# Kernel tuning notes

Hardware: AMD Instinct MI355X
Metric: run time of the kernel (lower is better)

## Reference

```python
import jax, jax.numpy as jnp
import numpy as np

DIM = 1024
NUM_HEADS = 16
HEAD_DIM = DIM // NUM_HEADS
BINDING_BIAS = 0.5
SCALE = HEAD_DIM ** -0.5


def setup_inputs() -> dict:
    key = jax.random.key(0)
    ks = jax.random.split(key, 10)
    B, S, D = 2, 2048, DIM
    std = D ** -0.5
    return {
        "x": jax.random.normal(ks[0], (B, S, D), jnp.float32),
        "binding_matrix": jax.random.uniform(ks[1], (S, S), jnp.float32),
        "Wq": jax.random.normal(ks[2], (D, D), jnp.float32) * std,
        "bq": jnp.zeros((D,), jnp.float32),
        "Wk": jax.random.normal(ks[3], (D, D), jnp.float32) * std,
        "bk": jnp.zeros((D,), jnp.float32),
        "Wv": jax.random.normal(ks[4], (D, D), jnp.float32) * std,
        "bv": jnp.zeros((D,), jnp.float32),
        "Wo": jax.random.normal(ks[5], (D, D), jnp.float32) * std,
        "bo": jnp.zeros((D,), jnp.float32),
    }


def reference(x, binding_matrix, Wq, bq, Wk, bk, Wv, bv, Wo, bo):
    B, S, D = x.shape
    H, Hd = NUM_HEADS, HEAD_DIM
    # projections -> [B, H, S, Hd]
    q = (x @ Wq + bq).reshape(B, S, H, Hd).transpose(0, 2, 1, 3)
    k = (x @ Wk + bk).reshape(B, S, H, Hd).transpose(0, 2, 1, 3)
    v = (x @ Wv + bv).reshape(B, S, H, Hd).transpose(0, 2, 1, 3)
    # scores [B, H, S, S] with additive binding bias
    attn = jnp.einsum("bhqd,bhkd->bhqk", q, k) * SCALE
    attn = attn + BINDING_BIAS * binding_matrix[None, None, :, :]
    attn = jax.nn.softmax(attn, axis=-1)
    out = jnp.einsum("bhqk,bhkd->bhqd", attn, v)
    out = out.transpose(0, 2, 1, 3).reshape(B, S, D)
    return out @ Wo + bo
```

## Files before the change

### kernel.cpp

```cpp
#include <hip/hip_runtime.h>

#define DEV static __device__ __forceinline__

typedef __attribute__((ext_vector_type(4))) float f32x4;
typedef __attribute__((ext_vector_type(8))) __bf16 bfv8;
typedef __attribute__((ext_vector_type(8))) short s8v;
typedef __attribute__((ext_vector_type(4))) short s4v;

DEV short f2bf(float f) {
    unsigned u = __float_as_uint(f);
    u = (u + 0x7fffu + ((u >> 16) & 1u)) >> 16;
    return (short)u;
}
DEV float bf2f(short s) { return __uint_as_float(((unsigned)(unsigned short)s) << 16); }

DEV void gload16(const void* g, void* l) {
    __builtin_amdgcn_global_load_lds(
        (const __attribute__((address_space(1))) void*)g,
        (__attribute__((address_space(3))) void*)l, 16, 0, 0);
}

DEV f32x4 mfma16(bfv8 a, bfv8 b, f32x4 c) {
    return __builtin_amdgcn_mfma_f32_16x16x32_bf16(a, b, c, 0, 0, 0);
}

DEV float max3f(float a, float b, float c) {
    float d;
    asm("v_max3_f32 %0, %1, %2, %3" : "=v"(d) : "v"(a), "v"(b), "v"(c));
    return d;
}
DEV unsigned cvtpk(float lo, float hi) {
    unsigned w;
    asm("v_cvt_pk_bf16_f32 %0, %1, %2" : "=v"(w) : "v"(lo), "v"(hi));
    return w;
}

DEV bfv8 ldsfrag(const short* base, int row, int slog) {
    int sp = slog ^ (row & 7);
    return *reinterpret_cast<const bfv8*>(base + row * 64 + sp * 8);
}

__global__ void k_cvt(const float* __restrict__ in, short* __restrict__ out, float s) {
    int i = blockIdx.x * blockDim.x + threadIdx.x;
    const float4* p = (const float4*)in + (size_t)i * 2;
    float4 a = p[0], b = p[1];
    s8v o;
    o[0] = f2bf(a.x * s); o[1] = f2bf(a.y * s); o[2] = f2bf(a.z * s); o[3] = f2bf(a.w * s);
    o[4] = f2bf(b.x * s); o[5] = f2bf(b.y * s); o[6] = f2bf(b.z * s); o[7] = f2bf(b.w * s);
    reinterpret_cast<s8v*>(out)[i] = o;
}

__global__ void k_cvtb(const float* __restrict__ in, short* __restrict__ out, float s) {
    int i = blockIdx.x * blockDim.x + threadIdx.x;
    int ktn = i >> 11, q = i & 2047;
    const float4* p = reinterpret_cast<const float4*>(in + (size_t)q * 2048 + ktn * 16);
    float4 a = p[0], b = p[1], cc = p[2], d = p[3];
    s8v o0, o1;
    o0[0] = f2bf(a.x * s); o0[1] = f2bf(a.y * s); o0[2] = f2bf(a.z * s); o0[3] = f2bf(a.w * s);
    o0[4] = f2bf(b.x * s); o0[5] = f2bf(b.y * s); o0[6] = f2bf(b.z * s); o0[7] = f2bf(b.w * s);
    o1[0] = f2bf(cc.x * s); o1[1] = f2bf(cc.y * s); o1[2] = f2bf(cc.z * s); o1[3] = f2bf(cc.w * s);
    o1[4] = f2bf(d.x * s); o1[5] = f2bf(d.y * s); o1[6] = f2bf(d.z * s); o1[7] = f2bf(d.w * s);
    s8v* dst = reinterpret_cast<s8v*>(out + (size_t)i * 16);
    dst[0] = o0; dst[1] = o1;
}

__global__ void k_transpose4(
    const float* __restrict__ W0, const float* __restrict__ W1,
    const float* __restrict__ W2, const float* __restrict__ W3,
    short* __restrict__ T0, short* __restrict__ T1,
    short* __restrict__ T2, short* __restrict__ T3, float s0)
{
    __shared__ float tl[32][33];
    const int z = blockIdx.z;
    const float* W = z == 0 ? W0 : z == 1 ? W1 : z == 2 ? W2 : W3;
    short* Wt = z == 0 ? T0 : z == 1 ? T1 : z == 2 ? T2 : T3;
    const float s = z == 0 ? s0 : 1.f;
    int tx = threadIdx.x & 31, ty = threadIdx.x >> 5;
    int nb = blockIdx.x * 32, kb = blockIdx.y * 32;
#pragma unroll
    for (int i = 0; i < 4; i++)
        tl[ty + i * 8][tx] = W[(kb + ty + i * 8) * 1024 + nb + tx];
    __syncthreads();
#pragma unroll
    for (int i = 0; i < 4; i++)
        Wt[(nb + ty + i * 8) * 1024 + kb + tx] = f2bf(tl[tx][ty + i * 8] * s);
}

template <int EPI>
DEV void gemm_store(f32x4 a4, int gr, int gc, const float* bias, float bscale,
                    void* outp)
{
    const float bvl = bias[gc] * bscale;
    const int h = gc >> 6, d = gc & 63;
    if (EPI == 2) {
        float* O = (float*)outp;
#pragma unroll
        for (int r = 0; r < 4; r++) O[(gr + r) * 1024 + gc] = a4[r] + bvl;
    } else {
        const int b = gr >> 11, sr = gr & 2047;
        short* O = (short*)outp;
        if (EPI == 0) {
            int base = ((b * 16 + h) * 2048 + sr) * 64 + d;
#pragma unroll
            for (int r = 0; r < 4; r++) O[base + r * 64] = f2bf(a4[r] + bvl);
        } else {
            s4v vv;
#pragma unroll
            for (int r = 0; r < 4; r++) vv[r] = f2bf(a4[r] + bvl);
            const int s6 = sr & 63;
            const int qp = (sr & ~63) | (s6 & 35) | ((s6 & 12) << 1) | ((s6 & 16) >> 2);
            *reinterpret_cast<s4v*>(O + ((b * 16 + h) * 64 + d) * 2048 + qp) = vv;
        }
    }
}

template <int EPI>
DEV void gemm_body(const short* __restrict__ A, const short* __restrict__ Bt,
                   const float* __restrict__ bias, void* __restrict__ outp,
                   float bscale, int row0, int col0, short* As, short* Bs)
{
    const int t = threadIdx.x, lane = t & 63;
    const int wv = t >> 6, wr = wv >> 1, wc = wv & 1;
    const int g = lane >> 4, c = lane & 15;

    const f32x4 z4 = {0.f, 0.f, 0.f, 0.f};
    f32x4 acc[2][4];
#pragma unroll
    for (int m = 0; m < 2; m++)
#pragma unroll
        for (int n = 0; n < 4; n++) acc[m][n] = z4;

    for (int kt = 0; kt < 16; ++kt) {
        const int k0 = kt * 64;
        const short* Ag = A + row0 * 1024 + k0;
        const short* Bg = Bt + col0 * 1024 + k0;
#pragma unroll
        for (int j = 0; j < 2; j++) {
            int idx = j * 256 + t;
            int row = idx >> 3, sp = idx & 7, sl = sp ^ (row & 7);
            gload16(Ag + row * 1024 + sl * 8, As + idx * 8);
        }
#pragma unroll
        for (int j = 0; j < 4; j++) {
            int idx = j * 256 + t;
            int row = idx >> 3, sp = idx & 7, sl = sp ^ (row & 7);
            gload16(Bg + row * 1024 + sl * 8, Bs + idx * 8);
        }
        __syncthreads();

        bfv8 af[2][2], bfr[4][2];
#pragma unroll
        for (int m = 0; m < 2; m++)
#pragma unroll
            for (int ks = 0; ks < 2; ks++)
                af[m][ks] = ldsfrag(As, wr * 32 + m * 16 + c, ks * 4 + g);
#pragma unroll
        for (int n = 0; n < 4; n++)
#pragma unroll
            for (int ks = 0; ks < 2; ks++)
                bfr[n][ks] = ldsfrag(Bs, wc * 64 + n * 16 + c, ks * 4 + g);
        __builtin_amdgcn_s_setprio(1);
#pragma unroll
        for (int m = 0; m < 2; m++)
#pragma unroll
            for (int n = 0; n < 4; n++)
#pragma unroll
                for (int ks = 0; ks < 2; ks++)
                    acc[m][n] = mfma16(af[m][ks], bfr[n][ks], acc[m][n]);
        __builtin_amdgcn_s_setprio(0);
        __syncthreads();
    }

#pragma unroll
    for (int n = 0; n < 4; n++) {
        const int gc = col0 + wc * 64 + n * 16 + c;
#pragma unroll
        for (int m = 0; m < 2; m++)
            gemm_store<EPI>(acc[m][n], row0 + wr * 32 + m * 16 + g * 4, gc,
                            bias, bscale, outp);
    }
}

template <int EPI>
DEV void gemm_body128(const short* __restrict__ A, const short* __restrict__ Bt,
                      const float* __restrict__ bias, void* __restrict__ outp,
                      float bscale, int row0, int col0, short* As, short* Bs)
{
    const int t = threadIdx.x, lane = t & 63;
    const int wv = t >> 6, wr = wv >> 1, wc = wv & 1;
    const int g = lane >> 4, c = lane & 15;

    const f32x4 z4 = {0.f, 0.f, 0.f, 0.f};
    f32x4 acc[4][4];
#pragma unroll
    for (int m = 0; m < 4; m++)
#pragma unroll
        for (int n = 0; n < 4; n++) acc[m][n] = z4;

    for (int kt = 0; kt < 16; ++kt) {
        const int k0 = kt * 64;
        const short* Ag = A + row0 * 1024 + k0;
        const short* Bg = Bt + col0 * 1024 + k0;
#pragma unroll
        for (int j = 0; j < 4; j++) {
            int idx = j * 256 + t;
            int row = idx >> 3, sp = idx & 7, sl = sp ^ (row & 7);
            gload16(Ag + row * 1024 + sl * 8, As + idx * 8);
            gload16(Bg + row * 1024 + sl * 8, Bs + idx * 8);
        }
        __syncthreads();

        bfv8 af[4][2], bfr[4][2];
#pragma unroll
        for (int m = 0; m < 4; m++)
#pragma unroll
            for (int ks = 0; ks < 2; ks++)
                af[m][ks] = ldsfrag(As, wr * 64 + m * 16 + c, ks * 4 + g);
#pragma unroll
        for (int n = 0; n < 4; n++)
#pragma unroll
            for (int ks = 0; ks < 2; ks++)
                bfr[n][ks] = ldsfrag(Bs, wc * 64 + n * 16 + c, ks * 4 + g);
        __builtin_amdgcn_s_setprio(1);
#pragma unroll
        for (int m = 0; m < 4; m++)
#pragma unroll
            for (int n = 0; n < 4; n++)
#pragma unroll
                for (int ks = 0; ks < 2; ks++)
                    acc[m][n] = mfma16(af[m][ks], bfr[n][ks], acc[m][n]);
        __builtin_amdgcn_s_setprio(0);
        __syncthreads();
    }

#pragma unroll
    for (int n = 0; n < 4; n++) {
        const int gc = col0 + wc * 64 + n * 16 + c;
#pragma unroll
        for (int m = 0; m < 4; m++)
            gemm_store<EPI>(acc[m][n], row0 + wr * 64 + m * 16 + g * 4, gc,
                            bias, bscale, outp);
    }
}

__global__ __launch_bounds__(256, 2) void k_gemm3(
    const short* __restrict__ A,
    const short* __restrict__ WqT, const short* __restrict__ WkT, const short* __restrict__ WvT,
    const float* __restrict__ bq, const float* __restrict__ bk, const float* __restrict__ bv,
    short* __restrict__ Qs, short* __restrict__ Kst, short* __restrict__ Vts, float scq)
{
    __shared__ alignas(16) short As[128 * 64];
    __shared__ alignas(16) short Bs[128 * 64];
    const int which = blockIdx.y >> 3;
    const int col0 = (blockIdx.y & 7) * 128;
    const int row0 = blockIdx.x * 128;
    if (which == 0)
        gemm_body128<0>(A, WqT, bq, Qs, scq, row0, col0, As, Bs);
    else if (which == 1)
        gemm_body128<0>(A, WkT, bk, Kst, 1.f, row0, col0, As, Bs);
    else
        gemm_body128<1>(A, WvT, bv, Vts, 1.f, row0, col0, As, Bs);
}

__global__ __launch_bounds__(256, 2) void k_gemmO(
    const short* __restrict__ A, const short* __restrict__ Bt,
    const float* __restrict__ bias, float* __restrict__ outp)
{
    __shared__ alignas(16) short As[64 * 64];
    __shared__ alignas(16) short Bs[128 * 64];
    gemm_body<2>(A, Bt, bias, outp, 1.f, blockIdx.x * 64, blockIdx.y * 128, As, Bs);
}

__global__ __launch_bounds__(1024, 4) void k_attn(
    const short* __restrict__ Q, const short* __restrict__ K,
    const short* __restrict__ Vt, const short* __restrict__ bbt,
    short* __restrict__ Ob)
{
    __shared__ alignas(16) short Ks[2][64 * 64];
    __shared__ alignas(16) short Vs[2][64 * 64];
    const int t = threadIdx.x, lane = t & 63;
    const int wv = t >> 6, g = lane >> 4, c = lane & 15;
    const int qt = blockIdx.x, bh = blockIdx.y;
    const int b = bh >> 4, h = bh & 15;
    const short* Qb = Q + bh * 2048 * 64;
    const short* Kb = K + bh * 2048 * 64;
    const short* Vb = Vt + bh * 64 * 2048;
    const int q0 = qt * 256 + wv * 16;

    bfv8 qf[2];
#pragma unroll
    for (int ks = 0; ks < 2; ks++)
        qf[ks] = *reinterpret_cast<const bfv8*>(Qb + (q0 + c) * 64 + ks * 32 + g * 8);

    const f32x4 z4 = {0.f, 0.f, 0.f, 0.f};
    f32x4 oa[4];
#pragma unroll
    for (int nd = 0; nd < 4; nd++) oa[nd] = z4;
    f32x4 lacc = z4;
    float mrun = 20.0f;

    s8v ob_;
#pragma unroll
    for (int i = 0; i < 8; i++) ob_[i] = (short)0x3F80;
    const bfv8 ones = __builtin_bit_cast(bfv8, ob_);

    const bool isK = t < 512;
    const int sidx = isK ? t : t - 512;
    const int srow = sidx >> 3, ssl = ((sidx & 7) ^ (srow & 7)) * 8;
    const short* sp_ = isK ? (Kb + srow * 64 + ssl) : (Vb + srow * 2048 + ssl);
    const int sinc = isK ? 4096 : 64;
    const int dst8 = sidx * 8;
    const short* bbp = bbt + (size_t)(q0 + c) * 16 + 4 * g;

    const int cx = c & 7;
    const int fofs0 = c * 128 + ((g ^ cx) << 4);
    const int fofs1 = c * 128 + (((4 + g) ^ cx) << 4);

    gload16(sp_, isK ? &Ks[0][dst8] : &Vs[0][dst8]);
    sp_ += sinc;
    s4v bn[4];
#pragma unroll
    for (int n = 0; n < 4; n++)
        bn[n] = *reinterpret_cast<const s4v*>(bbp + n * 32768);
    bbp += 131072;
    __syncthreads();

    for (int kt = 0; kt < 32; ++kt) {
        const int cur = kt & 1;
        f32x4 cb[4];
#pragma unroll
        for (int n = 0; n < 4; n++)
#pragma unroll
            for (int r = 0; r < 4; r++) cb[n][r] = bf2f(bn[n][r]);
        if (kt < 31) {
            const int nb = cur ^ 1;
            gload16(sp_, isK ? &Ks[nb][dst8] : &Vs[nb][dst8]);
            sp_ += sinc;
#pragma unroll
            for (int n = 0; n < 4; n++)
                bn[n] = *reinterpret_cast<const s4v*>(bbp + n * 32768);
            bbp += 131072;
        }

        const char* Kc = (const char*)&Ks[cur][0];
        const char* Vc = (const char*)&Vs[cur][0];

        f32x4 sc[4];
        __builtin_amdgcn_s_setprio(1);
#pragma unroll
        for (int n = 0; n < 4; n++) {
            bfv8 k0 = *reinterpret_cast<const bfv8*>(Kc + fofs0 + n * 2048);
            bfv8 k1 = *reinterpret_cast<const bfv8*>(Kc + fofs1 + n * 2048);
            sc[n] = mfma16(k0, qf[0], cb[n]);
            sc[n] = mfma16(k1, qf[1], sc[n]);
        }
        __builtin_amdgcn_s_setprio(0);

#pragma unroll
        for (int n = 0; n < 4; n++)
#pragma unroll
            for (int r = 0; r < 4; r++)
                sc[n][r] = __builtin_amdgcn_exp2f(sc[n][r] - mrun);

        unsigned w0[4], w1[4];
#pragma unroll
        for (int n = 0; n < 4; n++) {
            w0[n] = cvtpk(sc[n][0], sc[n][1]);
            w1[n] = cvtpk(sc[n][2], sc[n][3]);
        }
        typedef struct { unsigned a, b, c2, d; } u4;
        u4 q0w; q0w.a = w0[0]; q0w.b = w1[0]; q0w.c2 = w0[1]; q0w.d = w1[1];
        u4 q1w; q1w.a = w0[2]; q1w.b = w1[2]; q1w.c2 = w0[3]; q1w.d = w1[3];
        const bfv8 pf0 = __builtin_bit_cast(bfv8, q0w);
        const bfv8 pf1 = __builtin_bit_cast(bfv8, q1w);

        __builtin_amdgcn_s_setprio(1);
#pragma unroll
        for (int nd = 0; nd < 4; nd++) {
            bfv8 v0 = *reinterpret_cast<const bfv8*>(Vc + fofs0 + nd * 2048);
            bfv8 v1 = *reinterpret_cast<const bfv8*>(Vc + fofs1 + nd * 2048);
            oa[nd] = mfma16(v0, pf0, oa[nd]);
            oa[nd] = mfma16(v1, pf1, oa[nd]);
        }
        lacc = mfma16(ones, pf0, lacc);
        lacc = mfma16(ones, pf1, lacc);
        __builtin_amdgcn_s_setprio(0);

        float t0 = fmaxf(max3f(sc[0][0], sc[0][1], sc[0][2]), sc[0][3]);
        float t1 = fmaxf(max3f(sc[1][0], sc[1][1], sc[1][2]), sc[1][3]);
        float t2 = fmaxf(max3f(sc[2][0], sc[2][1], sc[2][2]), sc[2][3]);
        float t3 = fmaxf(max3f(sc[3][0], sc[3][1], sc[3][2]), sc[3][3]);
        float pemax = fmaxf(max3f(t0, t1, t2), t3);
        if (!__all(pemax <= 2896.0f)) {
            float rmax = fmaxf(pemax, __shfl_xor(pemax, 16));
            rmax = fmaxf(rmax, __shfl_xor(rmax, 32));
            if (rmax > 2896.0f) {
                const float corr = 1.0f / rmax;
                mrun += __log2f(rmax);
#pragma unroll
                for (int nd = 0; nd < 4; nd++)
#pragma unroll
                    for (int r = 0; r < 4; r++) oa[nd][r] *= corr;
#pragma unroll
                for (int r = 0; r < 4; r++) lacc[r] *= corr;
            }
        }
        __syncthreads();
    }

    const float rl = 1.0f / lacc[0];
    const size_t orow = (size_t)(b * 2048 + q0 + c);
#pragma unroll
    for (int nd = 0; nd < 4; nd++) {
        s4v st;
#pragma unroll
        for (int r = 0; r < 4; r++) st[r] = f2bf(oa[nd][r] * rl);
        *reinterpret_cast<s4v*>(Ob + orow * 1024 + h * 64 + nd * 16 + 4 * g) = st;
    }
}

extern "C" void kernel_launch(void* const* d_in, const int* in_sizes, int n_in,
                              void* d_out, int out_size, void* d_ws, size_t ws_size,
                              hipStream_t stream)
{
    (void)in_sizes; (void)n_in; (void)out_size; (void)ws_size;
    const float* x    = (const float*)d_in[0];
    const float* bind = (const float*)d_in[1];
    const float* Wq   = (const float*)d_in[2];
    const float* bq   = (const float*)d_in[3];
    const float* Wk   = (const float*)d_in[4];
    const float* bk   = (const float*)d_in[5];
    const float* Wv   = (const float*)d_in[6];
    const float* bv   = (const float*)d_in[7];
    const float* Wo   = (const float*)d_in[8];
    const float* bo   = (const float*)d_in[9];

    char* ws = (char*)d_ws;
    const size_t MB = (size_t)1 << 20;
    short* xb   = (short*)(ws + 0 * MB);
    short* Wqt  = (short*)(ws + 8 * MB);
    short* Wkt  = (short*)(ws + 10 * MB);
    short* Wvt  = (short*)(ws + 12 * MB);
    short* Wot  = (short*)(ws + 14 * MB);
    short* bbm  = (short*)(ws + 16 * MB);
    short* Qs   = (short*)(ws + 24 * MB);
    short* Kst  = (short*)(ws + 32 * MB);
    short* Vts  = (short*)(ws + 40 * MB);
    short* Obuf = (short*)(ws + 48 * MB);

    const float LOG2E = 1.4426950408889634f;
    const float SCQ = 0.125f * LOG2E;
    const float SCB = 0.5f * LOG2E;

    k_cvt<<<2048, 256, 0, stream>>>(x, xb, 1.f);
    k_cvtb<<<1024, 256, 0, stream>>>(bind, bbm, SCB);
    k_transpose4<<<dim3(32, 32, 4), 256, 0, stream>>>(Wq, Wk, Wv, Wo,
                                                      Wqt, Wkt, Wvt, Wot, SCQ);
    k_gemm3<<<dim3(32, 24), 256, 0, stream>>>(xb, Wqt, Wkt, Wvt, bq, bk, bv,
                                              Qs, Kst, Vts, SCQ);
    k_attn<<<dim3(8, 32), 1024, 0, stream>>>(Qs, Kst, Vts, bbm, Obuf);
    k_gemmO<<<dim3(64, 8), 256, 0, stream>>>(Obuf, Wot, bo, (float*)d_out);
}
```

Before: 122.0 us.

## Double attention key tile to 128 and split K/V loads across all threads

The attention loop now handles 128 keys per iteration instead of 64, halving the iteration count and the number of block-wide barriers. Every thread now issues one K and one V global-to-LDS load per tile, instead of half the threads loading K and half loading V. The V shared-memory layout and swizzled fragment offsets are reworked for the wider tile. In exchange, LDS use doubles to 64KB per block and each thread holds more score and bias registers, which may lower occupancy or cause spills given the 1024-thread launch bound.

```diff
diff --git a/kernel.cpp b/kernel.cpp
--- a/kernel.cpp
+++ b/kernel.cpp
@@ -276,8 +276,8 @@
     const short* __restrict__ Vt, const short* __restrict__ bbt,
     short* __restrict__ Ob)
 {
-    __shared__ alignas(16) short Ks[2][64 * 64];
-    __shared__ alignas(16) short Vs[2][64 * 64];
+    __shared__ alignas(16) short Ks[2][128 * 64];
+    __shared__ alignas(16) short Vs[2][64 * 128];
     const int t = threadIdx.x, lane = t & 63;
     const int wv = t >> 6, g = lane >> 4, c = lane & 15;
     const int qt = blockIdx.x, bh = blockIdx.y;
@@ -304,93 +304,101 @@
     for (int i = 0; i < 8; i++) ob_[i] = (short)0x3F80;
     const bfv8 ones = __builtin_bit_cast(bfv8, ob_);
 
-    const bool isK = t < 512;
-    const int sidx = isK ? t : t - 512;
-    const int srow = sidx >> 3, ssl = ((sidx & 7) ^ (srow & 7)) * 8;
-    const short* sp_ = isK ? (Kb + srow * 64 + ssl) : (Vb + srow * 2048 + ssl);
-    const int sinc = isK ? 4096 : 64;
-    const int dst8 = sidx * 8;
+    const int krow = t >> 3, ksl = ((t & 7) ^ (krow & 7)) * 8;
+    const short* kp0 = Kb + krow * 64 + ksl;
+    const int vrow = t >> 4, vp_ = t & 15;
+    const int vcol = ((vp_ >> 3) * 8 + ((vp_ & 7) ^ (vrow & 7))) * 8;
+    const short* vp0 = Vb + vrow * 2048 + vcol;
+    const int dst8 = t * 8;
     const short* bbp = bbt + (size_t)(q0 + c) * 16 + 4 * g;
 
     const int cx = c & 7;
-    const int fofs0 = c * 128 + ((g ^ cx) << 4);
-    const int fofs1 = c * 128 + (((4 + g) ^ cx) << 4);
-
-    gload16(sp_, isK ? &Ks[0][dst8] : &Vs[0][dst8]);
-    sp_ += sinc;
-    s4v bn[4];
-#pragma unroll
-    for (int n = 0; n < 4; n++)
+    const int kofs0 = c * 128 + ((g ^ cx) << 4);
+    const int kofs1 = c * 128 + (((4 + g) ^ cx) << 4);
+    int vofs[4];
+#pragma unroll
+    for (int j = 0; j < 4; j++)
+        vofs[j] = c * 256 + (((((j & 1) * 4 + g) ^ cx) + 8 * (j >> 1)) << 4);
+
+    gload16(kp0, &Ks[0][dst8]);
+    gload16(vp0, &Vs[0][dst8]);
+    kp0 += 8192; vp0 += 128;
+    s4v bn[8];
+#pragma unroll
+    for (int n = 0; n < 8; n++)
         bn[n] = *reinterpret_cast<const s4v*>(bbp + n * 32768);
-    bbp += 131072;
+    bbp += 262144;
     __syncthreads();
 
-    for (int kt = 0; kt < 32; ++kt) {
+    for (int kt = 0; kt < 16; ++kt) {
         const int cur = kt & 1;
-        f32x4 cb[4];
-#pragma unroll
-        for (int n = 0; n < 4; n++)
-#pragma unroll
-            for (int r = 0; r < 4; r++) cb[n][r] = bf2f(bn[n][r]);
-        if (kt < 31) {
+        const char* Kc = (const char*)&Ks[cur][0];
+        f32x4 sc[8];
+        __builtin_amdgcn_s_setprio(1);
+#pragma unroll
+        for (int n = 0; n < 8; n++) {
+            f32x4 cb;
+#pragma unroll
+            for (int r = 0; r < 4; r++) cb[r] = bf2f(bn[n][r]);
+            bfv8 k0 = *reinterpret_cast<const bfv8*>(Kc + kofs0 + n * 2048);
+            bfv8 k1 = *reinterpret_cast<const bfv8*>(Kc + kofs1 + n * 2048);
+            sc[n] = mfma16(k0, qf[0], cb);
+            sc[n] = mfma16(k1, qf[1], sc[n]);
+        }
+        __builtin_amdgcn_s_setprio(0);
+
+        if (kt < 15) {
             const int nb = cur ^ 1;
-            gload16(sp_, isK ? &Ks[nb][dst8] : &Vs[nb][dst8]);
-            sp_ += sinc;
-#pragma unroll
-            for (int n = 0; n < 4; n++)
+            gload16(kp0, &Ks[nb][dst8]);
+            gload16(vp0, &Vs[nb][dst8]);
+            kp0 += 8192; vp0 += 128;
+#pragma unroll
+            for (int n = 0; n < 8; n++)
                 bn[n] = *reinterpret_cast<const s4v*>(bbp + n * 32768);
-            bbp += 131072;
-        }
-
-        const char* Kc = (const char*)&Ks[cur][0];
-        const char* Vc = (const char*)&Vs[cur][0];
-
-        f32x4 sc[4];
-        __builtin_amdgcn_s_setprio(1);
-#pragma unroll
-        for (int n = 0; n < 4; n++) {
-            bfv8 k0 = *reinterpret_cast<const bfv8*>(Kc + fofs0 + n * 2048);
-            bfv8 k1 = *reinterpret_cast<const bfv8*>(Kc + fofs1 + n * 2048);
-            sc[n] = mfma16(k0, qf[0], cb[n]);
-            sc[n] = mfma16(k1, qf[1], sc[n]);
-        }
-        __builtin_amdgcn_s_setprio(0);
-
-#pragma unroll
-        for (int n = 0; n < 4; n++)
+            bbp += 262144;
+        }
+
+#pragma unroll
+        for (int n = 0; n < 8; n++)
 #pragma unroll
             for (int r = 0; r < 4; r++)
                 sc[n][r] = __builtin_amdgcn_exp2f(sc[n][r] - mrun);
 
-        unsigned w0[4], w1[4];
-#pragma unroll
-        for (int n = 0; n < 4; n++) {
+        unsigned w0[8], w1[8];
+#pragma unroll
+        for (int n = 0; n < 8; n++) {
             w0[n] = cvtpk(sc[n][0], sc[n][1]);
             w1[n] = cvtpk(sc[n][2], sc[n][3]);
         }
         typedef struct { unsigned a, b, c2, d; } u4;
-        u4 q0w; q0w.a = w0[0]; q0w.b = w1[0]; q0w.c2 = w0[1]; q0w.d = w1[1];
-        u4 q1w; q1w.a = w0[2]; q1w.b = w1[2]; q1w.c2 = w0[3]; q1w.d = w1[3];
-        const bfv8 pf0 = __builtin_bit_cast(bfv8, q0w);
-        const bfv8 pf1 = __builtin_bit_cast(bfv8, q1w);
-
+        bfv8 pf[4];
+#pragma unroll
+        for (int j = 0; j < 4; j++) {
+            u4 qw; qw.a = w0[2 * j]; qw.b = w1[2 * j];
+            qw.c2 = w0[2 * j + 1]; qw.d = w1[2 * j + 1];
+            pf[j] = __builtin_bit_cast(bfv8, qw);
+        }
+
+        const char* Vc = (const char*)&Vs[cur][0];
         __builtin_amdgcn_s_setprio(1);
 #pragma unroll
         for (int nd = 0; nd < 4; nd++) {
-            bfv8 v0 = *reinterpret_cast<const bfv8*>(Vc + fofs0 + nd * 2048);
-            bfv8 v1 = *reinterpret_cast<const bfv8*>(Vc + fofs1 + nd * 2048);
-            oa[nd] = mfma16(v0, pf0, oa[nd]);
-            oa[nd] = mfma16(v1, pf1, oa[nd]);
-        }
-        lacc = mfma16(ones, pf0, lacc);
-        lacc = mfma16(ones, pf1, lacc);
+#pragma unroll
+            for (int j = 0; j < 4; j++) {
+                bfv8 vf = *reinterpret_cast<const bfv8*>(Vc + vofs[j] + nd * 4096);
+                oa[nd] = mfma16(vf, pf[j], oa[nd]);
+            }
+        }
+#pragma unroll
+        for (int j = 0; j < 4; j++) lacc = mfma16(ones, pf[j], lacc);
         __builtin_amdgcn_s_setprio(0);
 
-        float t0 = fmaxf(max3f(sc[0][0], sc[0][1], sc[0][2]), sc[0][3]);
-        float t1 = fmaxf(max3f(sc[1][0], sc[1][1], sc[1][2]), sc[1][3]);
-        float t2 = fmaxf(max3f(sc[2][0], sc[2][1], sc[2][2]), sc[2][3]);
-        float t3 = fmaxf(max3f(sc[3][0], sc[3][1], sc[3][2]), sc[3][3]);
-        float pemax = fmaxf(max3f(t0, t1, t2), t3);
+        float pemax = 0.f;
+#pragma unroll
+        for (int n = 0; n < 8; n++) {
+            float tn = fmaxf(max3f(sc[n][0], sc[n][1], sc[n][2]), sc[n][3]);
+            pemax = fmaxf(pemax, tn);
+        }
         if (!__all(pemax <= 2896.0f)) {
             float rmax = fmaxf(pemax, __shfl_xor(pemax, 16));
             rmax = fmaxf(rmax, __shfl_xor(rmax, 32));
```

New measurement: 123.6 us. About the same (+1.4%).

## Double-buffer LDS tiles in projection GEMMs to overlap loads with MFMA

Applied to the files above, without the earlier changes.

Both GEMM bodies (QKV projection and output projection) now use two LDS buffers per operand. The next K-tile is prefetched with global_load_lds while MFMAs run on the current tile, and per-thread source pointers are precomputed and advanced instead of recomputed each iteration. This is meant to hide global-load latency behind compute. In exchange it doubles the GEMM kernels' shared-memory footprint, which may limit how many blocks fit per CU.

```diff
diff --git a/kernel.cpp b/kernel.cpp
--- a/kernel.cpp
+++ b/kernel.cpp
@@ -117,7 +117,8 @@
 template <int EPI>
 DEV void gemm_body(const short* __restrict__ A, const short* __restrict__ Bt,
                    const float* __restrict__ bias, void* __restrict__ outp,
-                   float bscale, int row0, int col0, short* As, short* Bs)
+                   float bscale, int row0, int col0, short (*As)[64 * 64],
+                   short (*Bs)[128 * 64])
 {
     const int t = threadIdx.x, lane = t & 63;
     const int wv = t >> 6, wr = wv >> 1, wc = wv & 1;
@@ -130,35 +131,46 @@
 #pragma unroll
         for (int n = 0; n < 4; n++) acc[m][n] = z4;
 
+    const short* Ap[2]; const short* Bp[4]; int Ad[2], Bd[4];
+#pragma unroll
+    for (int j = 0; j < 2; j++) {
+        int idx = j * 256 + t;
+        int row = idx >> 3, sl = ((idx & 7) ^ (row & 7)) * 8;
+        Ap[j] = A + row0 * 1024 + row * 1024 + sl;
+        Ad[j] = idx * 8;
+    }
+#pragma unroll
+    for (int j = 0; j < 4; j++) {
+        int idx = j * 256 + t;
+        int row = idx >> 3, sl = ((idx & 7) ^ (row & 7)) * 8;
+        Bp[j] = Bt + col0 * 1024 + row * 1024 + sl;
+        Bd[j] = idx * 8;
+    }
+    auto stage = [&](int buf) {
+#pragma unroll
+        for (int j = 0; j < 2; j++) { gload16(Ap[j], &As[buf][Ad[j]]); Ap[j] += 64; }
+#pragma unroll
+        for (int j = 0; j < 4; j++) { gload16(Bp[j], &Bs[buf][Bd[j]]); Bp[j] += 64; }
+    };
+
+    stage(0);
+    __syncthreads();
+
     for (int kt = 0; kt < 16; ++kt) {
-        const int k0 = kt * 64;
-        const short* Ag = A + row0 * 1024 + k0;
-        const short* Bg = Bt + col0 * 1024 + k0;
-#pragma unroll
-        for (int j = 0; j < 2; j++) {
-            int idx = j * 256 + t;
-            int row = idx >> 3, sp = idx & 7, sl = sp ^ (row & 7);
-            gload16(Ag + row * 1024 + sl * 8, As + idx * 8);
-        }
-#pragma unroll
-        for (int j = 0; j < 4; j++) {
-            int idx = j * 256 + t;
-            int row = idx >> 3, sp = idx & 7, sl = sp ^ (row & 7);
-            gload16(Bg + row * 1024 + sl * 8, Bs + idx * 8);
-        }
-        __syncthreads();
+        const int cur = kt & 1;
+        if (kt < 15) stage(cur ^ 1);
 
         bfv8 af[2][2], bfr[4][2];
 #pragma unroll
         for (int m = 0; m < 2; m++)
 #pragma unroll
             for (int ks = 0; ks < 2; ks++)
-                af[m][ks] = ldsfrag(As, wr * 32 + m * 16 + c, ks * 4 + g);
+                af[m][ks] = ldsfrag(As[cur], wr * 32 + m * 16 + c, ks * 4 + g);
 #pragma unroll
         for (int n = 0; n < 4; n++)
 #pragma unroll
             for (int ks = 0; ks < 2; ks++)
-                bfr[n][ks] = ldsfrag(Bs, wc * 64 + n * 16 + c, ks * 4 + g);
+                bfr[n][ks] = ldsfrag(Bs[cur], wc * 64 + n * 16 + c, ks * 4 + g);
         __builtin_amdgcn_s_setprio(1);
 #pragma unroll
         for (int m = 0; m < 2; m++)
@@ -184,7 +196,8 @@
 template <int EPI>
 DEV void gemm_body128(const short* __restrict__ A, const short* __restrict__ Bt,
                       const float* __restrict__ bias, void* __restrict__ outp,
-                      float bscale, int row0, int col0, short* As, short* Bs)
+                      float bscale, int row0, int col0, short (*As)[128 * 64],
+                      short (*Bs)[128 * 64])
 {
     const int t = threadIdx.x, lane = t & 63;
     const int wv = t >> 6, wr = wv >> 1, wc = wv & 1;
@@ -197,30 +210,41 @@
 #pragma unroll
         for (int n = 0; n < 4; n++) acc[m][n] = z4;
 
+    const short* Ap[4]; const short* Bp[4]; int Cd[4];
+#pragma unroll
+    for (int j = 0; j < 4; j++) {
+        int idx = j * 256 + t;
+        int row = idx >> 3, sl = ((idx & 7) ^ (row & 7)) * 8;
+        Ap[j] = A + row0 * 1024 + row * 1024 + sl;
+        Bp[j] = Bt + col0 * 1024 + row * 1024 + sl;
+        Cd[j] = idx * 8;
+    }
+    auto stage = [&](int buf) {
+#pragma unroll
+        for (int j = 0; j < 4; j++) {
+            gload16(Ap[j], &As[buf][Cd[j]]); Ap[j] += 64;
+            gload16(Bp[j], &Bs[buf][Cd[j]]); Bp[j] += 64;
+        }
+    };
+
+    stage(0);
+    __syncthreads();
+
     for (int kt = 0; kt < 16; ++kt) {
-        const int k0 = kt * 64;
-        const short* Ag = A + row0 * 1024 + k0;
-        const short* Bg = Bt + col0 * 1024 + k0;
-#pragma unroll
-        for (int j = 0; j < 4; j++) {
-            int idx = j * 256 + t;
-            int row = idx >> 3, sp = idx & 7, sl = sp ^ (row & 7);
-            gload16(Ag + row * 1024 + sl * 8, As + idx * 8);
-            gload16(Bg + row * 1024 + sl * 8, Bs + idx * 8);
-        }
-        __syncthreads();
+        const int cur = kt & 1;
+        if (kt < 15) stage(cur ^ 1);
 
         bfv8 af[4][2], bfr[4][2];
 #pragma unroll
         for (int m = 0; m < 4; m++)
 #pragma unroll
             for (int ks = 0; ks < 2; ks++)
-                af[m][ks] = ldsfrag(As, wr * 64 + m * 16 + c, ks * 4 + g);
+                af[m][ks] = ldsfrag(As[cur], wr * 64 + m * 16 + c, ks * 4 + g);
 #pragma unroll
         for (int n = 0; n < 4; n++)
 #pragma unroll
             for (int ks = 0; ks < 2; ks++)
-                bfr[n][ks] = ldsfrag(Bs, wc * 64 + n * 16 + c, ks * 4 + g);
+                bfr[n][ks] = ldsfrag(Bs[cur], wc * 64 + n * 16 + c, ks * 4 + g);
         __builtin_amdgcn_s_setprio(1);
 #pragma unroll
         for (int m = 0; m < 4; m++)
@@ -249,8 +273,8 @@
     const float* __restrict__ bq, const float* __restrict__ bk, const float* __restrict__ bv,
     short* __restrict__ Qs, short* __restrict__ Kst, short* __restrict__ Vts, float scq)
 {
-    __shared__ alignas(16) short As[128 * 64];
-    __shared__ alignas(16) short Bs[128 * 64];
+    __shared__ alignas(16) short As[2][128 * 64];
+    __shared__ alignas(16) short Bs[2][128 * 64];
     const int which = blockIdx.y >> 3;
     const int col0 = (blockIdx.y & 7) * 128;
     const int row0 = blockIdx.x * 128;
@@ -266,8 +290,8 @@
     const short* __restrict__ A, const short* __restrict__ Bt,
     const float* __restrict__ bias, float* __restrict__ outp)
 {
-    __shared__ alignas(16) short As[64 * 64];
-    __shared__ alignas(16) short Bs[128 * 64];
+    __shared__ alignas(16) short As[2][64 * 64];
+    __shared__ alignas(16) short Bs[2][128 * 64];
     gemm_body<2>(A, Bt, bias, outp, 1.f, blockIdx.x * 64, blockIdx.y * 128, As, Bs);
 }
 
```

New measurement: 123.4 us. About the same (+1.1%).

## Process two 16-row query groups per wave in attention, halving block size

Applied to the files above, without the earlier changes.

Each wave of the attention kernel now handles 32 query rows (two 16-row groups) instead of 16, so each K and V fragment read from LDS feeds twice as many MFMAs. The block shrinks from 1024 to 512 threads, and every thread now stages both a K and a V chunk per tile. The binding-bias prefetch moves after the QK MFMAs. The aim is to cut LDS read traffic and barrier cost per unit of matrix work. In exchange, register pressure roughly doubles for accumulators and score tiles, which could lower occupancy or cause spills.

```diff
diff --git a/kernel.cpp b/kernel.cpp
--- a/kernel.cpp
+++ b/kernel.cpp
@@ -271,7 +271,7 @@
     gemm_body<2>(A, Bt, bias, outp, 1.f, blockIdx.x * 64, blockIdx.y * 128, As, Bs);
 }
 
-__global__ __launch_bounds__(1024, 4) void k_attn(
+__global__ __launch_bounds__(512, 4) void k_attn(
     const short* __restrict__ Q, const short* __restrict__ K,
     const short* __restrict__ Vt, const short* __restrict__ bbt,
     short* __restrict__ Ob)
@@ -285,18 +285,21 @@
     const short* Qb = Q + bh * 2048 * 64;
     const short* Kb = K + bh * 2048 * 64;
     const short* Vb = Vt + bh * 64 * 2048;
-    const int q0 = qt * 256 + wv * 16;
-
-    bfv8 qf[2];
-#pragma unroll
-    for (int ks = 0; ks < 2; ks++)
-        qf[ks] = *reinterpret_cast<const bfv8*>(Qb + (q0 + c) * 64 + ks * 32 + g * 8);
+    const int q0 = qt * 256 + wv * 32;
+
+    bfv8 qf[2][2];
+#pragma unroll
+    for (int grp = 0; grp < 2; grp++)
+#pragma unroll
+        for (int ks = 0; ks < 2; ks++)
+            qf[grp][ks] = *reinterpret_cast<const bfv8*>(
+                Qb + (q0 + 16 * grp + c) * 64 + ks * 32 + g * 8);
 
     const f32x4 z4 = {0.f, 0.f, 0.f, 0.f};
-    f32x4 oa[4];
-#pragma unroll
-    for (int nd = 0; nd < 4; nd++) oa[nd] = z4;
-    f32x4 lacc = z4;
+    f32x4 oa0[4], oa1[4];
+#pragma unroll
+    for (int nd = 0; nd < 4; nd++) { oa0[nd] = z4; oa1[nd] = z4; }
+    f32x4 lacc0 = z4, lacc1 = z4;
     float mrun = 20.0f;
 
     s8v ob_;
@@ -304,93 +307,116 @@
     for (int i = 0; i < 8; i++) ob_[i] = (short)0x3F80;
     const bfv8 ones = __builtin_bit_cast(bfv8, ob_);
 
-    const bool isK = t < 512;
-    const int sidx = isK ? t : t - 512;
-    const int srow = sidx >> 3, ssl = ((sidx & 7) ^ (srow & 7)) * 8;
-    const short* sp_ = isK ? (Kb + srow * 64 + ssl) : (Vb + srow * 2048 + ssl);
-    const int sinc = isK ? 4096 : 64;
-    const int dst8 = sidx * 8;
+    const int srow = t >> 3, ssl = ((t & 7) ^ (srow & 7)) * 8;
+    const short* kp = Kb + srow * 64 + ssl;
+    const short* vp = Vb + srow * 2048 + ssl;
+    const int dst8 = t * 8;
     const short* bbp = bbt + (size_t)(q0 + c) * 16 + 4 * g;
 
     const int cx = c & 7;
     const int fofs0 = c * 128 + ((g ^ cx) << 4);
     const int fofs1 = c * 128 + (((4 + g) ^ cx) << 4);
 
-    gload16(sp_, isK ? &Ks[0][dst8] : &Vs[0][dst8]);
-    sp_ += sinc;
-    s4v bn[4];
-#pragma unroll
-    for (int n = 0; n < 4; n++)
-        bn[n] = *reinterpret_cast<const s4v*>(bbp + n * 32768);
+    gload16(kp, &Ks[0][dst8]);
+    gload16(vp, &Vs[0][dst8]);
+    kp += 4096; vp += 64;
+    s4v bn[2][4];
+#pragma unroll
+    for (int grp = 0; grp < 2; grp++)
+#pragma unroll
+        for (int n = 0; n < 4; n++)
+            bn[grp][n] = *reinterpret_cast<const s4v*>(bbp + grp * 256 + n * 32768);
     bbp += 131072;
     __syncthreads();
 
     for (int kt = 0; kt < 32; ++kt) {
         const int cur = kt & 1;
-        f32x4 cb[4];
-#pragma unroll
-        for (int n = 0; n < 4; n++)
-#pragma unroll
-            for (int r = 0; r < 4; r++) cb[n][r] = bf2f(bn[n][r]);
         if (kt < 31) {
             const int nb = cur ^ 1;
-            gload16(sp_, isK ? &Ks[nb][dst8] : &Vs[nb][dst8]);
-            sp_ += sinc;
-#pragma unroll
-            for (int n = 0; n < 4; n++)
-                bn[n] = *reinterpret_cast<const s4v*>(bbp + n * 32768);
-            bbp += 131072;
+            gload16(kp, &Ks[nb][dst8]);
+            gload16(vp, &Vs[nb][dst8]);
+            kp += 4096; vp += 64;
         }
 
         const char* Kc = (const char*)&Ks[cur][0];
         const char* Vc = (const char*)&Vs[cur][0];
 
-        f32x4 sc[4];
+        f32x4 sc0[4], sc1[4];
         __builtin_amdgcn_s_setprio(1);
 #pragma unroll
         for (int n = 0; n < 4; n++) {
             bfv8 k0 = *reinterpret_cast<const bfv8*>(Kc + fofs0 + n * 2048);
             bfv8 k1 = *reinterpret_cast<const bfv8*>(Kc + fofs1 + n * 2048);
-            sc[n] = mfma16(k0, qf[0], cb[n]);
-            sc[n] = mfma16(k1, qf[1], sc[n]);
+            f32x4 cb0, cb1;
+#pragma unroll
+            for (int r = 0; r < 4; r++) {
+                cb0[r] = bf2f(bn[0][n][r]);
+                cb1[r] = bf2f(bn[1][n][r]);
+            }
+            sc0[n] = mfma16(k0, qf[0][0], cb0);
+            sc0[n] = mfma16(k1, qf[0][1], sc0[n]);
+            sc1[n] = mfma16(k0, qf[1][0], cb1);
+            sc1[n] = mfma16(k1, qf[1][1], sc1[n]);
         }
         __builtin_amdgcn_s_setprio(0);
 
+        if (kt < 31) {
+#pragma unroll
+            for (int grp = 0; grp < 2; grp++)
+#pragma unroll
+                for (int n = 0; n < 4; n++)
+                    bn[grp][n] = *reinterpret_cast<const s4v*>(
+                        bbp + grp * 256 + n * 32768);
+            bbp += 131072;
+        }
+
 #pragma unroll
         for (int n = 0; n < 4; n++)
 #pragma unroll
-            for (int r = 0; r < 4; r++)
-                sc[n][r] = __builtin_amdgcn_exp2f(sc[n][r] - mrun);
-
-        unsigned w0[4], w1[4];
-#pragma unroll
-        for (int n = 0; n < 4; n++) {
-            w0[n] = cvtpk(sc[n][0], sc[n][1]);
-            w1[n] = cvtpk(sc[n][2], sc[n][3]);
-        }
+            for (int r = 0; r < 4; r++) {
+                sc0[n][r] = __builtin_amdgcn_exp2f(sc0[n][r] - mrun);
+                sc1[n][r] = __builtin_amdgcn_exp2f(sc1[n][r] - mrun);
+            }
+
         typedef struct { unsigned a, b, c2, d; } u4;
-        u4 q0w; q0w.a = w0[0]; q0w.b = w1[0]; q0w.c2 = w0[1]; q0w.d = w1[1];
-        u4 q1w; q1w.a = w0[2]; q1w.b = w1[2]; q1w.c2 = w0[3]; q1w.d = w1[3];
-        const bfv8 pf0 = __builtin_bit_cast(bfv8, q0w);
-        const bfv8 pf1 = __builtin_bit_cast(bfv8, q1w);
+        u4 qa, qb, qc, qd;
+        qa.a = cvtpk(sc0[0][0], sc0[0][1]); qa.b = cvtpk(sc0[0][2], sc0[0][3]);
+        qa.c2 = cvtpk(sc0[1][0], sc0[1][1]); qa.d = cvtpk(sc0[1][2], sc0[1][3]);
+        qb.a = cvtpk(sc0[2][0], sc0[2][1]); qb.b = cvtpk(sc0[2][2], sc0[2][3]);
+        qb.c2 = cvtpk(sc0[3][0], sc0[3][1]); qb.d = cvtpk(sc0[3][2], sc0[3][3]);
+        qc.a = cvtpk(sc1[0][0], sc1[0][1]); qc.b = cvtpk(sc1[0][2], sc1[0][3]);
+        qc.c2 = cvtpk(sc1[1][0], sc1[1][1]); qc.d = cvtpk(sc1[1][2], sc1[1][3]);
+        qd.a = cvtpk(sc1[2][0], sc1[2][1]); qd.b = cvtpk(sc1[2][2], sc1[2][3]);
+        qd.c2 = cvtpk(sc1[3][0], sc1[3][1]); qd.d = cvtpk(sc1[3][2], sc1[3][3]);
+        const bfv8 pf00 = __builtin_bit_cast(bfv8, qa);
+        const bfv8 pf01 = __builtin_bit_cast(bfv8, qb);
+        const bfv8 pf10 = __builtin_bit_cast(bfv8, qc);
+        const bfv8 pf11 = __builtin_bit_cast(bfv8, qd);
 
         __builtin_amdgcn_s_setprio(1);
 #pragma unroll
         for (int nd = 0; nd < 4; nd++) {
             bfv8 v0 = *reinterpret_cast<const bfv8*>(Vc + fofs0 + nd * 2048);
             bfv8 v1 = *reinterpret_cast<const bfv8*>(Vc + fofs1 + nd * 2048);
-            oa[nd] = mfma16(v0, pf0, oa[nd]);
-            oa[nd] = mfma16(v1, pf1, oa[nd]);
-        }
-        lacc = mfma16(ones, pf0, lacc);
-        lacc = mfma16(ones, pf1, lacc);
+            oa0[nd] = mfma16(v0, pf00, oa0[nd]);
+            oa0[nd] = mfma16(v1, pf01, oa0[nd]);
+            oa1[nd] = mfma16(v0, pf10, oa1[nd]);
+            oa1[nd] = mfma16(v1, pf11, oa1[nd]);
+        }
+        lacc0 = mfma16(ones, pf00, lacc0);
+        lacc0 = mfma16(ones, pf01, lacc0);
+        lacc1 = mfma16(ones, pf10, lacc1);
+        lacc1 = mfma16(ones, pf11, lacc1);
         __builtin_amdgcn_s_setprio(0);
 
-        float t0 = fmaxf(max3f(sc[0][0], sc[0][1], sc[0][2]), sc[0][3]);
-        float t1 = fmaxf(max3f(sc[1][0], sc[1][1], sc[1][2]), sc[1][3]);
-        float t2 = fmaxf(max3f(sc[2][0], sc[2][1], sc[2][2]), sc[2][3]);
-        float t3 = fmaxf(max3f(sc[3][0], sc[3][1], sc[3][2]), sc[3][3]);
-        float pemax = fmaxf(max3f(t0, t1, t2), t3);
+        float pemax = 0.f;
+#pragma unroll
+        for (int n = 0; n < 4; n++) {
+            pemax = fmaxf(pemax, fmaxf(max3f(sc0[n][0], sc0[n][1], sc0[n][2]),
+                                       sc0[n][3]));
+            pemax = fmaxf(pemax, fmaxf(max3f(sc1[n][0], sc1[n][1], sc1[n][2]),
+                                       sc1[n][3]));
+        }
         if (!__all(pemax <= 2896.0f)) {
             float rmax = fmaxf(pemax, __shfl_xor(pemax, 16));
             rmax = fmaxf(rmax, __shfl_xor(rmax, 32));
@@ -400,22 +426,31 @@
 #pragma unroll
                 for (int nd = 0; nd < 4; nd++)
 #pragma unroll
-                    for (int r = 0; r < 4; r++) oa[nd][r] *= corr;
-#pragma unroll
-                for (int r = 0; r < 4; r++) lacc[r] *= corr;
+                    for (int r = 0; r < 4; r++) {
+                        oa0[nd][r] *= corr;
+                        oa1[nd][r] *= corr;
+                    }
+#pragma unroll
+                for (int r = 0; r < 4; r++) { lacc0[r] *= corr; lacc1[r] *= corr; }
             }
         }
         __syncthreads();
     }
 
-    const float rl = 1.0f / lacc[0];
-    const size_t orow = (size_t)(b * 2048 + q0 + c);
+    const float rl0 = 1.0f / lacc0[0];
+    const float rl1 = 1.0f / lacc1[0];
+    const size_t row0_ = (size_t)(b * 2048 + q0 + c);
+    const size_t row1_ = row0_ + 16;
 #pragma unroll
     for (int nd = 0; nd < 4; nd++) {
-        s4v st;
-#pragma unroll
-        for (int r = 0; r < 4; r++) st[r] = f2bf(oa[nd][r] * rl);
-        *reinterpret_cast<s4v*>(Ob + orow * 1024 + h * 64 + nd * 16 + 4 * g) = st;
+        s4v s0, s1;
+#pragma unroll
+        for (int r = 0; r < 4; r++) {
+            s0[r] = f2bf(oa0[nd][r] * rl0);
+            s1[r] = f2bf(oa1[nd][r] * rl1);
+        }
+        *reinterpret_cast<s4v*>(Ob + row0_ * 1024 + h * 64 + nd * 16 + 4 * g) = s0;
+        *reinterpret_cast<s4v*>(Ob + row1_ * 1024 + h * 64 + nd * 16 + 4 * g) = s1;
     }
 }
 
@@ -458,6 +493,6 @@
                                                       Wqt, Wkt, Wvt, Wot, SCQ);
     k_gemm3<<<dim3(32, 24), 256, 0, stream>>>(xb, Wqt, Wkt, Wvt, bq, bk, bv,
                                               Qs, Kst, Vts, SCQ);
-    k_attn<<<dim3(8, 32), 1024, 0, stream>>>(Qs, Kst, Vts, bbm, Obuf);
+    k_attn<<<dim3(8, 32), 512, 0, stream>>>(Qs, Kst, Vts, bbm, Obuf);
     k_gemmO<<<dim3(64, 8), 256, 0, stream>>>(Obuf, Wot, bo, (float*)d_out);
 }
```

Measured after the change: 158.0 us. 1.3x slower.
